# Kernel tuning notes

Measured on AMD Instinct MI355X. Metric: run time of the kernel, lower is better.

Reference implementation:

```python
import jax, jax.numpy as jnp
import numpy as np

BN_EPS = 1e-5

def _conv(x, w, b=None, pad=0):
    # x: NCHW, w: OIHW
    y = jax.lax.conv_general_dilated(x, w, (1, 1), [(pad, pad), (pad, pad)],
                                     dimension_numbers=('NCHW', 'OIHW', 'NCHW'))
    if b is not None:
        y = y + b[None, :, None, None]
    return y

def setup_inputs() -> dict:
    key = jax.random.key(0)
    ks = jax.random.split(key, 16)
    B, C, H, W = 8, 10, 128, 128
    IN_DIM = 256
    inp = {
        'f_node': jax.random.normal(ks[0], (B, C, H, W), jnp.float32),
        'h_node0': jax.random.normal(ks[1], (B, C, H, W), jnp.float32),
        'h_node1': jax.random.normal(ks[2], (B, C, H, W), jnp.float32),
        'p_nodes': jax.random.normal(ks[3], (6, B, C, H, W), jnp.float32),
        'xf': jax.random.normal(ks[4], (B, IN_DIM, H, W), jnp.float32),
        # Comp_att: 1x1 conv (2*C -> 1) + bias, then sigmoid
        'att_w': jax.random.normal(ks[5], (1, 2 * C, 1, 1), jnp.float32) * 0.1,
        'att_b': jnp.zeros((1,), jnp.float32),
        # Composition: 3x3 conv (2*C -> C), no bias; BatchNorm (eval-mode stats)
        'rel_w': jax.random.normal(ks[6], (C, 2 * C, 3, 3), jnp.float32) * 0.1,
        'bn_gamma': jnp.ones((C,), jnp.float32),
        'bn_beta': jnp.zeros((C,), jnp.float32),
        'bn_mean': jnp.zeros((C,), jnp.float32),
        'bn_var': jnp.ones((C,), jnp.float32),
        # ConvGRU (1x1 kernels): gates conv (2*C -> 2*C), candidate conv (2*C -> C)
        'gates_w': jax.random.normal(ks[7], (2 * C, 2 * C, 1, 1), jnp.float32) * 0.1,
        'gates_b': jnp.zeros((2 * C,), jnp.float32),
        'can_w': jax.random.normal(ks[8], (C, 2 * C, 1, 1), jnp.float32) * 0.1,
        'can_b': jnp.zeros((C,), jnp.float32),
    }
    return inp

def reference(f_node, h_node0, h_node1, p_nodes, xf,
              att_w, att_b, rel_w, bn_gamma, bn_beta, bn_mean, bn_var,
              gates_w, gates_b, can_w, can_b):
    C = f_node.shape[1]
    # --- Comp_att: sigmoid(1x1 conv over concat of children) -> [B,1,H,W]
    comp_att = jax.nn.sigmoid(_conv(jnp.concatenate([h_node0, h_node1], axis=1), att_w, att_b))
    # --- Composition: sum over children of ReLU(BN(conv3x3(cat[parent, child*att])))
    inv_std = bn_gamma / jnp.sqrt(bn_var + BN_EPS)
    def relation(child):
        y = _conv(jnp.concatenate([f_node, child * comp_att], axis=1), rel_w, pad=1)
        y = (y - bn_mean[None, :, None, None]) * inv_std[None, :, None, None] + bn_beta[None, :, None, None]
        return jax.nn.relu(y)
    comp_h = relation(h_node0) + relation(h_node1)
    # --- ConvGRU update (single step, 1x1 convs): input=comp_h, hidden=f_node
    combined = jnp.concatenate([comp_h, f_node], axis=1)
    gates = _conv(combined, gates_w, gates_b)
    reset = jax.nn.sigmoid(gates[:, :C])
    update = jax.nn.sigmoid(gates[:, C:])
    cand = jnp.tanh(_conv(jnp.concatenate([comp_h, reset * f_node], axis=1), can_w, can_b))
    f_node_new = (1.0 - update) * f_node + update * cand
    return (f_node_new, comp_att)
```

## Files before the change

### kernel.cpp

```cpp
#include <hip/hip_runtime.h>

#define B_   8
#define C_   10
#define H_   128
#define W_   128
#define HWSZ (H_ * W_)
#define CHW  (C_ * HWSZ)

#define TS   16
#define HL   18
#define HST  19
#define HSZ  (HL * HL)
#define NTHREADS 256

#define WOFF_W3 0
#define WOFF_BI 1800
#define WOFF_AW 1810
#define WOFF_AB 1830
#define WOFF_GW 1832
#define WOFF_GB 2232
#define WOFF_CW 2252
#define WOFF_CB 2452

__device__ __forceinline__ float sigm(float x)  { return 1.0f / (1.0f + __expf(-x)); }
__device__ __forceinline__ float tanh_(float x) { return 1.0f - 2.0f / (__expf(2.0f * x) + 1.0f); }

__global__ __launch_bounds__(256) void prep_kernel(
    const float* __restrict__ attw, const float* __restrict__ attb,
    const float* __restrict__ relw,
    const float* __restrict__ gamma, const float* __restrict__ beta,
    const float* __restrict__ mean,  const float* __restrict__ var,
    const float* __restrict__ gw, const float* __restrict__ gb,
    const float* __restrict__ cw, const float* __restrict__ cb,
    float* __restrict__ ws)
{
    const int tid = threadIdx.x;
    for (int i = tid; i < 1800; i += 256) {
        const int g20 = i / 20, j = i - g20 * 20;
        const int tap = g20 / 10, ci = g20 - tap * 10;
        const int c   = (j < 10) ? j : j - 10;
        const int cin = (j < 10) ? ci : 10 + ci;
        const float sc = gamma[c] * rsqrtf(var[c] + 1e-5f);
        ws[WOFF_W3 + i] = relw[(c * 20 + cin) * 9 + tap] * sc;
    }
    if (tid < 10) {
        const float sc = gamma[tid] * rsqrtf(var[tid] + 1e-5f);
        ws[WOFF_BI + tid] = beta[tid] - mean[tid] * sc;
        ws[WOFF_CB + tid] = cb[tid];
    }
    if (tid < 20) {
        ws[WOFF_AW + tid] = attw[tid];
        ws[WOFF_GB + tid] = gb[tid];
    }
    if (tid == 0) ws[WOFF_AB] = attb[0];
    for (int i = tid; i < 400; i += 256) {
        const int ic = i / 20, o = i - ic * 20;
        ws[WOFF_GW + i] = gw[o * 20 + ic];
    }
    for (int i = tid; i < 200; i += 256) {
        const int ic = i / 10, c = i - ic * 10;
        ws[WOFF_CW + i] = cw[c * 20 + ic];
    }
}

__global__ __launch_bounds__(NTHREADS) void fused_graph_kernel(
    const float* __restrict__ f_g,
    const float* __restrict__ h0_g,
    const float* __restrict__ h1_g,
    const float* __restrict__ ws,
    float* __restrict__ out_f,
    float* __restrict__ out_att)
{
    __shared__ float4 sIn[C_][HL * HST];

    const int tid = threadIdx.x;
    const int bx = blockIdx.x, by = blockIdx.y, b = blockIdx.z;

    float aw[20];
    #pragma unroll
    for (int i = 0; i < 20; i++) aw[i] = ws[WOFF_AW + i];
    const float ab = ws[WOFF_AB];

    const int gy0 = by * TS - 1, gx0 = bx * TS - 1;
    for (int p = tid; p < HSZ; p += NTHREADS) {
        const int hy = p / HL, hx = p - hy * HL;
        const int gy = gy0 + hy, gx = gx0 + hx;
        const int q = hy * HST + hx;
        if (gy >= 0 && gy < H_ && gx >= 0 && gx < W_) {
            const int base = b * CHW + gy * W_ + gx;
            float fv[10], h0v[10], h1v[10];
            float acc = ab;
            #pragma unroll
            for (int ci = 0; ci < 10; ci++) {
                fv[ci]  = f_g [base + ci * HWSZ];
                h0v[ci] = h0_g[base + ci * HWSZ];
                h1v[ci] = h1_g[base + ci * HWSZ];
                acc += aw[ci] * h0v[ci] + aw[10 + ci] * h1v[ci];
            }
            const float att = sigm(acc);
            #pragma unroll
            for (int ci = 0; ci < 10; ci++)
                sIn[ci][q] = make_float4(fv[ci], h0v[ci] * att, h1v[ci] * att, att);
        } else {
            #pragma unroll
            for (int ci = 0; ci < 10; ci++)
                sIn[ci][q] = make_float4(0.f, 0.f, 0.f, 0.f);
        }
    }
    __syncthreads();

    const int ly = tid >> 4, lx = tid & 15;
    const int hc = (ly + 1) * HST + (lx + 1);

    float accf[10], acc0[10], acc1[10];
    #pragma unroll
    for (int c = 0; c < 10; c++) { accf[c] = 0.f; acc0[c] = 0.f; acc1[c] = 0.f; }

    #pragma unroll 1
    for (int tap = 0; tap < 9; tap++) {
        const int hi = hc + (tap / 3 - 1) * HST + (tap - (tap / 3) * 3 - 1);
        #pragma unroll
        for (int ci = 0; ci < 10; ci++) {
            const float4 v = sIn[ci][hi];
            const float* __restrict__ wp = ws + WOFF_W3 + (tap * 10 + ci) * 20;
            #pragma unroll
            for (int c = 0; c < 10; c++) {
                accf[c] += wp[c]      * v.x;
                acc0[c] += wp[10 + c] * v.y;
                acc1[c] += wp[10 + c] * v.z;
            }
        }
    }

    float ch[10], fc[10], attv = 0.f;
    #pragma unroll
    for (int c = 0; c < 10; c++) {
        const float4 cv = sIn[c][hc];
        fc[c] = cv.x;
        if (c == 0) attv = cv.w;
        const float bi = ws[WOFF_BI + c];
        ch[c] = fmaxf(accf[c] + acc0[c] + bi, 0.f) + fmaxf(accf[c] + acc1[c] + bi, 0.f);
    }

    float g[20];
    #pragma unroll
    for (int o = 0; o < 20; o++) g[o] = ws[WOFF_GB + o];
    #pragma unroll
    for (int i = 0; i < 10; i++) {
        #pragma unroll
        for (int o = 0; o < 20; o++)
            g[o] += ch[i] * ws[WOFF_GW + i * 20 + o] + fc[i] * ws[WOFF_GW + (10 + i) * 20 + o];
    }
    float cd[10];
    #pragma unroll
    for (int c = 0; c < 10; c++) cd[c] = ws[WOFF_CB + c];
    #pragma unroll
    for (int i = 0; i < 10; i++) {
        const float rf = sigm(g[i]) * fc[i];
        #pragma unroll
        for (int c = 0; c < 10; c++)
            cd[c] += ch[i] * ws[WOFF_CW + i * 10 + c] + rf * ws[WOFF_CW + (10 + i) * 10 + c];
    }

    const int gy = by * TS + ly, gx = bx * TS + lx;
    #pragma unroll
    for (int c = 0; c < 10; c++) {
        const float u = sigm(g[10 + c]);
        out_f[((b * C_ + c) * H_ + gy) * W_ + gx] = (1.f - u) * fc[c] + u * tanh_(cd[c]);
    }
    out_att[(b * H_ + gy) * W_ + gx] = attv;
}

extern "C" void kernel_launch(void* const* d_in, const int* in_sizes, int n_in,
                              void* d_out, int out_size, void* d_ws, size_t ws_size,
                              hipStream_t stream) {
    (void)in_sizes; (void)n_in; (void)ws_size; (void)out_size;
    const float* f   = (const float*)d_in[0];
    const float* h0  = (const float*)d_in[1];
    const float* h1  = (const float*)d_in[2];
    const float* aw  = (const float*)d_in[5];
    const float* ab  = (const float*)d_in[6];
    const float* rw  = (const float*)d_in[7];
    const float* gam = (const float*)d_in[8];
    const float* bet = (const float*)d_in[9];
    const float* mea = (const float*)d_in[10];
    const float* var = (const float*)d_in[11];
    const float* gw  = (const float*)d_in[12];
    const float* gb  = (const float*)d_in[13];
    const float* cw  = (const float*)d_in[14];
    const float* cb  = (const float*)d_in[15];

    float* wsf     = (float*)d_ws;
    float* out_f   = (float*)d_out;
    float* out_att = out_f + (B_ * C_ * H_ * W_);

    prep_kernel<<<1, 256, 0, stream>>>(aw, ab, rw, gam, bet, mea, var, gw, gb, cw, cb, wsf);

    dim3 grid(W_ / TS, H_ / TS, B_);
    fused_graph_kernel<<<grid, dim3(NTHREADS), 0, stream>>>(f, h0, h1, wsf, out_f, out_att);
}
```

Measured before the change: 241.8 us.

## Drop weight-prep kernel and read raw weights directly in fused kernel

Removes the separate single-block prep kernel that reordered and BN-folded the weights into workspace. The fused kernel now reads the original OIHW conv weights and the GRU weights with strided indices, and applies the BN scale and bias after the convolution. The shared-memory row padding (stride 19) is also removed in favour of a dense 18-wide tile. This saves one kernel launch and its serialization, at the cost of strided, non-contiguous scalar weight loads in the inner loop and possible LDS bank conflicts.

```diff
diff --git a/kernel.cpp b/kernel.cpp
--- a/kernel.cpp
+++ b/kernel.cpp
@@ -9,83 +9,44 @@
 
 #define TS   16
 #define HL   18
-#define HST  19
 #define HSZ  (HL * HL)
 #define NTHREADS 256
 
-#define WOFF_W3 0
-#define WOFF_BI 1800
-#define WOFF_AW 1810
-#define WOFF_AB 1830
-#define WOFF_GW 1832
-#define WOFF_GB 2232
-#define WOFF_CW 2252
-#define WOFF_CB 2452
-
 __device__ __forceinline__ float sigm(float x)  { return 1.0f / (1.0f + __expf(-x)); }
 __device__ __forceinline__ float tanh_(float x) { return 1.0f - 2.0f / (__expf(2.0f * x) + 1.0f); }
-
-__global__ __launch_bounds__(256) void prep_kernel(
-    const float* __restrict__ attw, const float* __restrict__ attb,
-    const float* __restrict__ relw,
-    const float* __restrict__ gamma, const float* __restrict__ beta,
-    const float* __restrict__ mean,  const float* __restrict__ var,
-    const float* __restrict__ gw, const float* __restrict__ gb,
-    const float* __restrict__ cw, const float* __restrict__ cb,
-    float* __restrict__ ws)
-{
-    const int tid = threadIdx.x;
-    for (int i = tid; i < 1800; i += 256) {
-        const int g20 = i / 20, j = i - g20 * 20;
-        const int tap = g20 / 10, ci = g20 - tap * 10;
-        const int c   = (j < 10) ? j : j - 10;
-        const int cin = (j < 10) ? ci : 10 + ci;
-        const float sc = gamma[c] * rsqrtf(var[c] + 1e-5f);
-        ws[WOFF_W3 + i] = relw[(c * 20 + cin) * 9 + tap] * sc;
-    }
-    if (tid < 10) {
-        const float sc = gamma[tid] * rsqrtf(var[tid] + 1e-5f);
-        ws[WOFF_BI + tid] = beta[tid] - mean[tid] * sc;
-        ws[WOFF_CB + tid] = cb[tid];
-    }
-    if (tid < 20) {
-        ws[WOFF_AW + tid] = attw[tid];
-        ws[WOFF_GB + tid] = gb[tid];
-    }
-    if (tid == 0) ws[WOFF_AB] = attb[0];
-    for (int i = tid; i < 400; i += 256) {
-        const int ic = i / 20, o = i - ic * 20;
-        ws[WOFF_GW + i] = gw[o * 20 + ic];
-    }
-    for (int i = tid; i < 200; i += 256) {
-        const int ic = i / 10, c = i - ic * 10;
-        ws[WOFF_CW + i] = cw[c * 20 + ic];
-    }
-}
 
 __global__ __launch_bounds__(NTHREADS) void fused_graph_kernel(
     const float* __restrict__ f_g,
     const float* __restrict__ h0_g,
     const float* __restrict__ h1_g,
-    const float* __restrict__ ws,
+    const float* __restrict__ attw_g,
+    const float* __restrict__ attb_g,
+    const float* __restrict__ relw_g,
+    const float* __restrict__ gamma_g,
+    const float* __restrict__ beta_g,
+    const float* __restrict__ mean_g,
+    const float* __restrict__ var_g,
+    const float* __restrict__ gw_g,
+    const float* __restrict__ gb_g,
+    const float* __restrict__ cw_g,
+    const float* __restrict__ cb_g,
     float* __restrict__ out_f,
     float* __restrict__ out_att)
 {
-    __shared__ float4 sIn[C_][HL * HST];
+    __shared__ float4 sIn[C_][HSZ];
 
     const int tid = threadIdx.x;
     const int bx = blockIdx.x, by = blockIdx.y, b = blockIdx.z;
 
     float aw[20];
     #pragma unroll
-    for (int i = 0; i < 20; i++) aw[i] = ws[WOFF_AW + i];
-    const float ab = ws[WOFF_AB];
+    for (int i = 0; i < 20; i++) aw[i] = attw_g[i];
+    const float ab = attb_g[0];
 
     const int gy0 = by * TS - 1, gx0 = bx * TS - 1;
     for (int p = tid; p < HSZ; p += NTHREADS) {
         const int hy = p / HL, hx = p - hy * HL;
         const int gy = gy0 + hy, gx = gx0 + hx;
-        const int q = hy * HST + hx;
         if (gy >= 0 && gy < H_ && gx >= 0 && gx < W_) {
             const int base = b * CHW + gy * W_ + gx;
             float fv[10], h0v[10], h1v[10];
@@ -100,17 +61,17 @@
             const float att = sigm(acc);
             #pragma unroll
             for (int ci = 0; ci < 10; ci++)
-                sIn[ci][q] = make_float4(fv[ci], h0v[ci] * att, h1v[ci] * att, att);
+                sIn[ci][p] = make_float4(fv[ci], h0v[ci] * att, h1v[ci] * att, att);
         } else {
             #pragma unroll
             for (int ci = 0; ci < 10; ci++)
-                sIn[ci][q] = make_float4(0.f, 0.f, 0.f, 0.f);
+                sIn[ci][p] = make_float4(0.f, 0.f, 0.f, 0.f);
         }
     }
     __syncthreads();
 
     const int ly = tid >> 4, lx = tid & 15;
-    const int hc = (ly + 1) * HST + (lx + 1);
+    const int hc = (ly + 1) * HL + (lx + 1);
 
     float accf[10], acc0[10], acc1[10];
     #pragma unroll
@@ -118,48 +79,54 @@
 
     #pragma unroll 1
     for (int tap = 0; tap < 9; tap++) {
-        const int hi = hc + (tap / 3 - 1) * HST + (tap - (tap / 3) * 3 - 1);
+        const int hi = hc + (tap / 3 - 1) * HL + (tap - (tap / 3) * 3 - 1);
+        const float* __restrict__ wt = relw_g + tap;
         #pragma unroll
         for (int ci = 0; ci < 10; ci++) {
             const float4 v = sIn[ci][hi];
-            const float* __restrict__ wp = ws + WOFF_W3 + (tap * 10 + ci) * 20;
             #pragma unroll
             for (int c = 0; c < 10; c++) {
-                accf[c] += wp[c]      * v.x;
-                acc0[c] += wp[10 + c] * v.y;
-                acc1[c] += wp[10 + c] * v.z;
+                accf[c] += wt[(c * 20 + ci)      * 9] * v.x;
+                const float wa = wt[(c * 20 + 10 + ci) * 9];
+                acc0[c] += wa * v.y;
+                acc1[c] += wa * v.z;
             }
         }
     }
 
-    float ch[10], fc[10], attv = 0.f;
+    float ch[10], fc[10], attv;
+    {
+        const float4 cv = sIn[0][hc];
+        fc[0] = cv.x; attv = cv.w;
+    }
+    #pragma unroll
+    for (int c = 1; c < 10; c++) fc[c] = sIn[c][hc].x;
     #pragma unroll
     for (int c = 0; c < 10; c++) {
-        const float4 cv = sIn[c][hc];
-        fc[c] = cv.x;
-        if (c == 0) attv = cv.w;
-        const float bi = ws[WOFF_BI + c];
-        ch[c] = fmaxf(accf[c] + acc0[c] + bi, 0.f) + fmaxf(accf[c] + acc1[c] + bi, 0.f);
+        const float sc = gamma_g[c] * rsqrtf(var_g[c] + 1e-5f);
+        const float bi = beta_g[c] - mean_g[c] * sc;
+        ch[c] = fmaxf((accf[c] + acc0[c]) * sc + bi, 0.f)
+              + fmaxf((accf[c] + acc1[c]) * sc + bi, 0.f);
     }
 
     float g[20];
     #pragma unroll
-    for (int o = 0; o < 20; o++) g[o] = ws[WOFF_GB + o];
+    for (int o = 0; o < 20; o++) g[o] = gb_g[o];
     #pragma unroll
     for (int i = 0; i < 10; i++) {
         #pragma unroll
         for (int o = 0; o < 20; o++)
-            g[o] += ch[i] * ws[WOFF_GW + i * 20 + o] + fc[i] * ws[WOFF_GW + (10 + i) * 20 + o];
+            g[o] += ch[i] * gw_g[o * 20 + i] + fc[i] * gw_g[o * 20 + 10 + i];
     }
     float cd[10];
     #pragma unroll
-    for (int c = 0; c < 10; c++) cd[c] = ws[WOFF_CB + c];
+    for (int c = 0; c < 10; c++) cd[c] = cb_g[c];
     #pragma unroll
     for (int i = 0; i < 10; i++) {
         const float rf = sigm(g[i]) * fc[i];
         #pragma unroll
         for (int c = 0; c < 10; c++)
-            cd[c] += ch[i] * ws[WOFF_CW + i * 10 + c] + rf * ws[WOFF_CW + (10 + i) * 10 + c];
+            cd[c] += ch[i] * cw_g[c * 20 + i] + rf * cw_g[c * 20 + 10 + i];
     }
 
     const int gy = by * TS + ly, gx = bx * TS + lx;
@@ -174,7 +141,7 @@
 extern "C" void kernel_launch(void* const* d_in, const int* in_sizes, int n_in,
                               void* d_out, int out_size, void* d_ws, size_t ws_size,
                               hipStream_t stream) {
-    (void)in_sizes; (void)n_in; (void)ws_size; (void)out_size;
+    (void)in_sizes; (void)n_in; (void)d_ws; (void)ws_size; (void)out_size;
     const float* f   = (const float*)d_in[0];
     const float* h0  = (const float*)d_in[1];
     const float* h1  = (const float*)d_in[2];
@@ -190,12 +157,10 @@
     const float* cw  = (const float*)d_in[14];
     const float* cb  = (const float*)d_in[15];
 
-    float* wsf     = (float*)d_ws;
     float* out_f   = (float*)d_out;
     float* out_att = out_f + (B_ * C_ * H_ * W_);
 
-    prep_kernel<<<1, 256, 0, stream>>>(aw, ab, rw, gam, bet, mea, var, gw, gb, cw, cb, wsf);
-
     dim3 grid(W_ / TS, H_ / TS, B_);
-    fused_graph_kernel<<<grid, dim3(NTHREADS), 0, stream>>>(f, h0, h1, wsf, out_f, out_att);
+    fused_graph_kernel<<<grid, dim3(NTHREADS), 0, stream>>>(
+        f, h0, h1, aw, ab, rw, gam, bet, mea, var, gw, gb, cw, cb, out_f, out_att);
 }
```

Measured after the change: 257.3 us. 1.06x slower.
